# Kernel optimization log

Hardware: AMD Instinct MI355X
Metric: run time of the kernel (lower is better)

## Reference

```python
import jax, jax.numpy as jnp
import numpy as np

B, IN, H, MID = 16384, 256, 512, 64
GRID_SIZE, ORDER = 5, 3
GRID_LO, GRID_HI = -1.0, 1.0
NB = GRID_SIZE + ORDER  # 8 spline basis functions per input feature
LN_EPS = 1e-5


def make_grid(in_features):
    h = (GRID_HI - GRID_LO) / GRID_SIZE
    g = np.arange(-ORDER, GRID_SIZE + ORDER + 1, dtype=np.float32) * h + GRID_LO
    return jnp.asarray(np.tile(g, (in_features, 1)))  # (in, grid_size + 2*order + 1)


def layer_norm(x, g, b):
    mu = jnp.mean(x, axis=-1, keepdims=True)
    var = jnp.var(x, axis=-1, keepdims=True)
    return (x - mu) * jax.lax.rsqrt(var + LN_EPS) * g + b


def b_splines(x, grid):
    # x: (B, in), grid: (in, G). Cox-de Boor recursion (efficient-kan convention).
    xe = x[:, :, None]
    bases = ((xe >= grid[:, :-1]) & (xe < grid[:, 1:])).astype(x.dtype)
    for k in range(1, ORDER + 1):
        left = (xe - grid[:, :-(k + 1)]) / (grid[:, k:-1] - grid[:, :-(k + 1)])
        right = (grid[:, k + 1:] - xe) / (grid[:, k + 1:] - grid[:, 1:-k])
        bases = left * bases[:, :, :-1] + right * bases[:, :, 1:]
    return bases  # (B, in, NB)


def kan_linear(x, base_w, spline_w, scaler, grid):
    # base path: silu(x) @ W_base^T ; spline path: B-spline bases contracted with scaled spline weights
    base = jax.nn.silu(x) @ base_w.T
    bs = b_splines(x, grid)
    spline = jnp.einsum('bik,oik->bo', bs, spline_w * scaler[:, :, None])
    return base + spline


def setup_inputs() -> dict:
    key = jax.random.key(0)
    ks = jax.random.split(key, 24)

    def n(k, shape, fan_in):
        return jax.random.normal(k, shape, dtype=jnp.float32) / np.sqrt(fan_in)

    H2 = 2 * H
    return {
        'x': jax.random.normal(ks[0], (B, IN), jnp.float32),
        'h_prev': jax.random.normal(ks[1], (B, H), jnp.float32),
        'ip_w': n(ks[2], (H, IN), IN), 'ip_b': jnp.zeros((H,), jnp.float32),
        'rg_w': n(ks[3], (H, H2), H2), 'rg_b': jnp.zeros((H,), jnp.float32),
        'rg_g': jnp.ones((H,), jnp.float32), 'rg_beta': jnp.zeros((H,), jnp.float32),
        'ug_w': n(ks[4], (H, H2), H2), 'ug_b': jnp.zeros((H,), jnp.float32),
        'ug_g': jnp.ones((H,), jnp.float32), 'ug_beta': jnp.zeros((H,), jnp.float32),
        'k1_base': n(ks[5], (MID, H2), H2),
        'k1_spline': n(ks[6], (MID, H2, NB), H2) * 0.1,
        'k1_scaler': n(ks[7], (MID, H2), H2) + 1.0,
        'grid1': make_grid(H2),
        'k2_base': n(ks[8], (H, MID), MID),
        'k2_spline': n(ks[9], (H, MID, NB), MID) * 0.1,
        'k2_scaler': n(ks[10], (H, MID), MID) + 1.0,
        'grid2': make_grid(MID),
        'cn_g': jnp.ones((H,), jnp.float32), 'cn_b': jnp.zeros((H,), jnp.float32),
        'rp_w': n(ks[11], (H, H2), H2), 'rp_b': jnp.zeros((H,), jnp.float32),
    }


def reference(x, h_prev, ip_w, ip_b, rg_w, rg_b, rg_g, rg_beta, ug_w, ug_b, ug_g, ug_beta,
              k1_base, k1_spline, k1_scaler, grid1, k2_base, k2_spline, k2_scaler, grid2,
              cn_g, cn_b, rp_w, rp_b):
    x_proj = x @ ip_w.T + ip_b
    combined = jnp.concatenate([x_proj, h_prev], axis=1)  # (B, 2H)
    # reset gate is computed in the original forward but never used; kept for faithfulness
    reset = jnp.tanh(layer_norm(combined @ rg_w.T + rg_b, rg_g, rg_beta))  # noqa: F841
    update = jax.nn.sigmoid(layer_norm(combined @ ug_w.T + ug_b, ug_g, ug_beta))
    # KAN candidate: [2H] -> 64 -> H
    mid = kan_linear(combined, k1_base, k1_spline, k1_scaler, grid1)
    h_cand = kan_linear(mid, k2_base, k2_spline, k2_scaler, grid2)
    residual = combined @ rp_w.T + rp_b
    h_cand = layer_norm(h_cand + residual, cn_g, cn_b)
    h_cand = layer_norm(h_cand, cn_g, cn_b)  # same LayerNorm applied twice, as in source
    h_cand = jax.nn.silu(h_cand)
    h_t = (1.0 - update) * h_prev + update * h_cand
    return h_t
```

## Files before the change

kernel.cpp:

```cpp
#include <hip/hip_runtime.h>
#include <hip/hip_bf16.h>

#define BATCH 16384

typedef __attribute__((ext_vector_type(8))) short short8;
typedef __attribute__((ext_vector_type(4))) float f32x4;

typedef const __attribute__((address_space(1))) uint* gas_t;
typedef __attribute__((address_space(3))) uint* las_t;

__device__ __forceinline__ void gl_lds16(const void* g, void* l) {
    __builtin_amdgcn_global_load_lds((gas_t)g, (las_t)l, 16, 0, 0);
}

__device__ __forceinline__ float bf2f(uint u) { union { uint u; float f; } v; v.u = u << 16; return v.f; }
__device__ __forceinline__ ushort f2bf(float f) {
    union { float f; uint u; } v; v.f = f;
    uint r = v.u + 0x7fffu + ((v.u >> 16) & 1u);
    return (ushort)(r >> 16);
}
__device__ __forceinline__ uint pack2(float a, float b) { return (uint)f2bf(a) | ((uint)f2bf(b) << 16); }
__device__ __forceinline__ uint pack_trunc(float lo, float hi) {
    return __builtin_amdgcn_perm(__float_as_uint(hi), __float_as_uint(lo), 0x07060302u);
}
__device__ __forceinline__ float sigmoidf_(float x) { return __builtin_amdgcn_rcpf(1.0f + __expf(-x)); }
__device__ __forceinline__ float siluf_(float x)    { return x * sigmoidf_(x); }

__device__ __forceinline__ void xcd_swz(int& bm, int& bn) {
    int lin = blockIdx.x + blockIdx.y * 128;
    int c = lin & 7, s = lin >> 3;
    bm = c * 16 + (s >> 2);
    bn = s & 3;
}

__device__ __forceinline__ void bases_packed(float x, float g0, float inv_h, uint o[4]) {
    float u = (x - g0) * inv_h;
    float fl = floorf(u);
    float f = u - fl;
    float f2 = f * f, f3 = f2 * f;
    float Ca = f3 * (1.0f / 6.0f);
    float Cb = (1.0f / 6.0f) + 0.5f * (f + f2 - f3);
    float Cc = (2.0f / 3.0f) + 0.5f * f3 - f2;
    float Cd = (1.0f / 6.0f) + 0.5f * (f2 - f) - f3 * (1.0f / 6.0f);
    int t0 = (int)fl;
    t0 = max(-8, min(t0, 19));
    uint dlo = pack_trunc(Cd, Cc);
    uint dhi = pack_trunc(Cb, Ca);
    unsigned long long D = (unsigned long long)dlo | ((unsigned long long)dhi << 32);
    int sp = t0 * 16 - 48;
    unsigned long long l1 = D << (sp & 63);
    unsigned long long r1 = D >> ((-sp) & 63);
    unsigned long long r2 = D >> ((64 - sp) & 63);
    unsigned long long l2 = D << ((sp - 64) & 63);
    unsigned long long lo = (sp >= 0) ? (sp < 64 ? l1 : 0ull) : (sp > -64 ? r1 : 0ull);
    unsigned long long hi = (sp > 0 && sp < 128) ? (sp < 64 ? r2 : l2) : 0ull;
    o[0] = (uint)lo; o[1] = (uint)(lo >> 32); o[2] = (uint)hi; o[3] = (uint)(hi >> 32);
}

__global__ __launch_bounds__(256) void prep_all(const float* __restrict__ hp,
                                                const float* __restrict__ ip_w, const float* __restrict__ ug_w,
                                                const float* __restrict__ rp,  const float* __restrict__ k2b,
                                                const float* __restrict__ k2s, const float* __restrict__ k2sc,
                                                const float* __restrict__ k1b, const float* __restrict__ k1s,
                                                const float* __restrict__ k1sc,
                                                ushort* __restrict__ acat,
                                                ushort* __restrict__ ipw, ushort* __restrict__ ugw,
                                                ushort* __restrict__ wcat, ushort* __restrict__ w1aug) {
    int t = blockIdx.x * 256 + threadIdx.x;
    if (t < 1048576) {
        int b = t >> 6, j = (t & 63) * 8;
        const float4* s = (const float4*)(hp + (size_t)b * 512 + j);
        float4 a = s[0], c = s[1];
        uint4 o; o.x = pack2(a.x, a.y); o.y = pack2(a.z, a.w); o.z = pack2(c.x, c.y); o.w = pack2(c.z, c.w);
        *(uint4*)(acat + (size_t)b * 1600 + 512 + j) = o;
        return;
    }
    t -= 1048576;
    if (t < 131072) { ipw[t] = f2bf(ip_w[t]); return; }
    t -= 131072;
    if (t < 524288) { ugw[t] = f2bf(ug_w[t]); return; }
    t -= 524288;
    if (t < 819200) {
        int n = t / 1600, c = t % 1600; float v;
        if (c < 1024) v = rp[n * 1024 + c];
        else if (c < 1088) v = k2b[n * 64 + (c - 1024)];
        else { int i = (c - 1088) >> 3, k = (c - 1088) & 7; v = k2s[(n * 64 + i) * 8 + k] * k2sc[n * 64 + i]; }
        wcat[t] = f2bf(v); return;
    }
    t -= 819200;
    if (t < 589824) {
        int n = t / 9216, c = t % 9216; float v;
        if (c < 1024) v = k1b[n * 1024 + c];
        else { int i = (c - 1024) >> 3, k = (c - 1024) & 7; v = k1s[(n * 1024 + i) * 8 + k] * k1sc[n * 1024 + i]; }
        w1aug[t] = f2bf(v);
    }
}

__global__ __launch_bounds__(256) void gemm_mfma(const ushort* __restrict__ A, int lda,
                                                 const ushort* __restrict__ Wt, int ldw,
                                                 const float* __restrict__ bias,
                                                 ushort* __restrict__ C, int ldc, int K) {
    __shared__ ushort As[2][128 * 64];
    __shared__ ushort Bs[2][128 * 64];
    const int tid = threadIdx.x;
    const int w = tid >> 6, lane = tid & 63;
    const int fr = lane & 15, fq = lane >> 4;
    int bm, bn; xcd_swz(bm, bn);
    const int m0 = bm * 128, n0 = bn * 128;
    const int wm = w & 1, wn = w >> 1;

    const int srow8 = lane >> 3;
    const int scol  = ((lane & 7) ^ srow8) << 3;
    const ushort* gA[4]; const ushort* gB[4]; int fa[4];
#pragma unroll
    for (int j = 0; j < 4; ++j) {
        int rowj = (j * 4 + w) * 8 + srow8;
        fa[j] = (j * 4 + w) * 512 + lane * 8;
        gA[j] = A  + (size_t)(m0 + rowj) * lda + scol;
        gB[j] = Wt + (size_t)(n0 + rowj) * ldw + scol;
    }
    const int nt = K / 64;
#pragma unroll
    for (int j = 0; j < 4; ++j) {
        gl_lds16(gA[j], &As[0][fa[j]]); gl_lds16(gB[j], &Bs[0][fa[j]]);
        gA[j] += 64; gB[j] += 64;
    }
    f32x4 acc[4][4] = {};
    int cur = 0;
    for (int t = 0; t < nt; ++t) {
        __syncthreads();
        if (t + 1 < nt) {
#pragma unroll
            for (int j = 0; j < 4; ++j) {
                gl_lds16(gA[j], &As[cur ^ 1][fa[j]]); gl_lds16(gB[j], &Bs[cur ^ 1][fa[j]]);
                gA[j] += 64; gB[j] += 64;
            }
        }
#pragma unroll
        for (int s = 0; s < 2; ++s) {
            const int csw = ((s * 4 + fq) ^ (fr & 7)) << 3;
            short8 af[4], bv[4];
#pragma unroll
            for (int mi = 0; mi < 4; ++mi)
                af[mi] = *(const short8*)(&As[cur][(wm * 64 + mi * 16 + fr) * 64 + csw]);
#pragma unroll
            for (int ni = 0; ni < 4; ++ni)
                bv[ni] = *(const short8*)(&Bs[cur][(wn * 64 + ni * 16 + fr) * 64 + csw]);
#pragma unroll
            for (int mi = 0; mi < 4; ++mi)
#pragma unroll
                for (int ni = 0; ni < 4; ++ni)
                    acc[mi][ni] = __builtin_amdgcn_mfma_f32_16x16x32_bf16(af[mi], bv[ni], acc[mi][ni], 0, 0, 0);
        }
        cur ^= 1;
    }
#pragma unroll
    for (int mi = 0; mi < 4; ++mi) {
#pragma unroll
        for (int ni = 0; ni < 4; ++ni) {
            int n = n0 + wn * 64 + ni * 16 + fr;
            float bvs = bias[n];
#pragma unroll
            for (int r = 0; r < 4; ++r) {
                int m = m0 + wm * 64 + mi * 16 + fq * 4 + r;
                C[(size_t)m * ldc + n] = f2bf(acc[mi][ni][r] + bvs);
            }
        }
    }
}

__global__ __launch_bounds__(256) void gemm_ip(const float* __restrict__ X,
                                               const ushort* __restrict__ Wt,
                                               const float* __restrict__ bias,
                                               ushort* __restrict__ acat) {
    __shared__ ushort As[2][128 * 64];
    __shared__ ushort Bs[2][128 * 64];
    const int tid = threadIdx.x;
    const int w = tid >> 6, lane = tid & 63;
    const int fr = lane & 15, fq = lane >> 4;
    int bm, bn; xcd_swz(bm, bn);
    const int m0 = bm * 128, n0 = bn * 128;
    const int wm = w & 1, wn = w >> 1;

    const int srow8 = lane >> 3;
    const int scol = ((lane & 7) ^ srow8) << 3;
    const ushort* gB[4]; int fa[4];
#pragma unroll
    for (int j = 0; j < 4; ++j) {
        int rowj = (j * 4 + w) * 8 + srow8;
        fa[j] = (j * 4 + w) * 512 + lane * 8;
        gB[j] = Wt + (size_t)(n0 + rowj) * 256 + scol;
    }
    const float* gA[4]; int ar[4];
#pragma unroll
    for (int j = 0; j < 4; ++j) {
        int rj = j * 32 + (tid >> 3);
        int lc = (tid & 7) ^ (rj & 7);
        ar[j] = rj * 64 + (tid & 7) * 8;
        gA[j] = X + (size_t)(m0 + rj) * 256 + lc * 8;
    }
    float4 va[4], vb[4];
#pragma unroll
    for (int j = 0; j < 4; ++j) { gl_lds16(gB[j], &Bs[0][fa[j]]); gB[j] += 64; }
#pragma unroll
    for (int j = 0; j < 4; ++j) { va[j] = *(const float4*)gA[j]; vb[j] = *(const float4*)(gA[j] + 4); gA[j] += 64; }
#pragma unroll
    for (int j = 0; j < 4; ++j) {
        uint4 o; o.x = pack2(va[j].x, va[j].y); o.y = pack2(va[j].z, va[j].w);
        o.z = pack2(vb[j].x, vb[j].y); o.w = pack2(vb[j].z, vb[j].w);
        *(uint4*)&As[0][ar[j]] = o;
    }
    f32x4 acc[4][4] = {};
    int cur = 0;
    for (int t = 0; t < 4; ++t) {
        __syncthreads();
        if (t < 3) {
#pragma unroll
            for (int j = 0; j < 4; ++j) { gl_lds16(gB[j], &Bs[cur ^ 1][fa[j]]); gB[j] += 64; }
#pragma unroll
            for (int j = 0; j < 4; ++j) { va[j] = *(const float4*)gA[j]; vb[j] = *(const float4*)(gA[j] + 4); gA[j] += 64; }
        }
#pragma unroll
        for (int s = 0; s < 2; ++s) {
            const int csw = ((s * 4 + fq) ^ (fr & 7)) << 3;
            short8 af[4], bv[4];
#pragma unroll
            for (int mi = 0; mi < 4; ++mi)
                af[mi] = *(const short8*)(&As[cur][(wm * 64 + mi * 16 + fr) * 64 + csw]);
#pragma unroll
            for (int ni = 0; ni < 4; ++ni)
                bv[ni] = *(const short8*)(&Bs[cur][(wn * 64 + ni * 16 + fr) * 64 + csw]);
#pragma unroll
            for (int mi = 0; mi < 4; ++mi)
#pragma unroll
                for (int ni = 0; ni < 4; ++ni)
                    acc[mi][ni] = __builtin_amdgcn_mfma_f32_16x16x32_bf16(af[mi], bv[ni], acc[mi][ni], 0, 0, 0);
        }
        if (t < 3) {
#pragma unroll
            for (int j = 0; j < 4; ++j) {
                uint4 o; o.x = pack2(va[j].x, va[j].y); o.y = pack2(va[j].z, va[j].w);
                o.z = pack2(vb[j].x, vb[j].y); o.w = pack2(vb[j].z, vb[j].w);
                *(uint4*)&As[cur ^ 1][ar[j]] = o;
            }
        }
        cur ^= 1;
    }
#pragma unroll
    for (int mi = 0; mi < 4; ++mi) {
#pragma unroll
        for (int ni = 0; ni < 4; ++ni) {
            int n = n0 + wn * 64 + ni * 16 + fr;
            float bvs = bias[n];
#pragma unroll
            for (int r = 0; r < 4; ++r) {
                int m = m0 + wm * 64 + mi * 16 + fq * 4 + r;
                acat[(size_t)m * 1600 + n] = f2bf(acc[mi][ni][r] + bvs);
            }
        }
    }
}

__global__ __launch_bounds__(256) void kan1_mfma(const ushort* __restrict__ acat,
                                                 const ushort* __restrict__ w1aug,
                                                 const float* __restrict__ grid1,
                                                 ushort* __restrict__ midp) {
    __shared__ ushort As[2][64 * 64];
    __shared__ ushort Bs[2][64 * 64];
    const int tid = threadIdx.x;
    const int w = tid >> 6, lane = tid & 63;
    const int fr = lane & 15, fq = lane >> 4;
    const int m0 = blockIdx.x * 64;
    const int kb = blockIdx.y;
    const float g0 = grid1[0];
    const float inv_h = 1.0f / (grid1[1] - g0);

    const int srow = tid >> 3, sc = tid & 7;
    const int xr = srow & 7;
    const int lc8 = (sc ^ xr) << 3;
    const ushort* wB0  = w1aug + (size_t)srow * 9216 + lc8;
    const ushort* wB1  = w1aug + (size_t)(srow + 32) * 9216 + lc8;
    const int wpo = srow * 64 + lc8;
    const int wm = w & 1, wn = w >> 1;
    const int cB = kb * 128;
    const int bB = 1024 + kb * 1024;

    const ushort* aR0 = acat + (size_t)(m0 + srow) * 1600;
    const ushort* aR1 = acat + (size_t)(m0 + srow + 32) * 1600;

    uint4 sA0[2], sA1[2];
#pragma unroll
    for (int s = 0; s < 2; ++s) {
        sA0[s] = *(const uint4*)(aR0 + cB + s * 64 + sc * 8);
        sA1[s] = *(const uint4*)(aR1 + cB + s * 64 + sc * 8);
    }
    uint xa[16], xb[16];
#pragma unroll
    for (int bs = 0; bs < 16; ++bs) {
        xa[bs] = aR0[cB + bs * 8 + sc];
        xb[bs] = aR1[cB + bs * 8 + sc];
    }

    f32x4 acc[2][2] = {};
    auto stageB = [&](int c, int buf) {
        gl_lds16(wB0 + c, &Bs[buf][tid * 8]);
        gl_lds16(wB1 + c, &Bs[buf][2048 + tid * 8]);
    };
    auto stageAsilu = [&](int s, int buf) {
        uint r0[4] = {sA0[s].x, sA0[s].y, sA0[s].z, sA0[s].w};
        uint r1[4] = {sA1[s].x, sA1[s].y, sA1[s].z, sA1[s].w};
        uint o0[4], o1[4];
#pragma unroll
        for (int p = 0; p < 4; ++p) {
            o0[p] = pack_trunc(siluf_(bf2f(r0[p] & 0xffffu)), siluf_(bf2f(r0[p] >> 16)));
            o1[p] = pack_trunc(siluf_(bf2f(r1[p] & 0xffffu)), siluf_(bf2f(r1[p] >> 16)));
        }
        uint4 q0; q0.x = o0[0]; q0.y = o0[1]; q0.z = o0[2]; q0.w = o0[3];
        uint4 q1; q1.x = o1[0]; q1.y = o1[1]; q1.z = o1[2]; q1.w = o1[3];
        *(uint4*)&As[buf][wpo] = q0;
        *(uint4*)&As[buf][2048 + wpo] = q1;
    };
    auto stageAbases = [&](uint x0u, uint x1u, int buf) {
        uint o0[4], o1[4];
        bases_packed(bf2f(x0u), g0, inv_h, o0);
        bases_packed(bf2f(x1u), g0, inv_h, o1);
        uint4 q0; q0.x = o0[0]; q0.y = o0[1]; q0.z = o0[2]; q0.w = o0[3];
        uint4 q1; q1.x = o1[0]; q1.y = o1[1]; q1.z = o1[2]; q1.w = o1[3];
        *(uint4*)&As[buf][wpo] = q0;
        *(uint4*)&As[buf][2048 + wpo] = q1;
    };
    auto mfma_step = [&](int buf) {
        __builtin_amdgcn_s_setprio(1);
#pragma unroll
        for (int s2 = 0; s2 < 2; ++s2) {
            short8 af[2], bv[2];
#pragma unroll
            for (int mi = 0; mi < 2; ++mi) {
                int arow = wm * 32 + mi * 16 + fr;
                af[mi] = *(const short8*)(&As[buf][arow * 64 + (((s2 * 4 + fq) ^ (arow & 7)) << 3)]);
            }
#pragma unroll
            for (int ni = 0; ni < 2; ++ni) {
                int brow = wn * 32 + ni * 16 + fr;
                bv[ni] = *(const short8*)(&Bs[buf][brow * 64 + (((s2 * 4 + fq) ^ (brow & 7)) << 3)]);
            }
#pragma unroll
            for (int mi = 0; mi < 2; ++mi)
#pragma unroll
                for (int ni = 0; ni < 2; ++ni)
                    acc[mi][ni] = __builtin_amdgcn_mfma_f32_16x16x32_bf16(af[mi], bv[ni], acc[mi][ni], 0, 0, 0);
        }
        __builtin_amdgcn_s_setprio(0);
    };

    stageB(cB, 0); stageAsilu(0, 0);
    __syncthreads();
    stageB(cB + 64, 1); stageAsilu(1, 1);
    mfma_step(0);
    __syncthreads();
    stageB(bB, 0); stageAbases(xa[0], xb[0], 0);
    mfma_step(1);
#pragma unroll
    for (int bs = 0; bs < 15; ++bs) {
        __syncthreads();
        stageB(bB + (bs + 1) * 64, (bs + 1) & 1);
        stageAbases(xa[bs + 1], xb[bs + 1], (bs + 1) & 1);
        mfma_step(bs & 1);
    }
    __syncthreads();
    mfma_step(1);

    ushort* outp = midp + (size_t)kb * (BATCH * 64);
#pragma unroll
    for (int mi = 0; mi < 2; ++mi)
#pragma unroll
        for (int ni = 0; ni < 2; ++ni)
#pragma unroll
            for (int r = 0; r < 4; ++r)
                outp[(size_t)(m0 + wm * 32 + mi * 16 + fq * 4 + r) * 64 + wn * 32 + ni * 16 + fr] = f2bf(acc[mi][ni][r]);
}

__global__ __launch_bounds__(256) void bs2_kernel(const ushort* __restrict__ midp,
                                                  const float* __restrict__ grid2,
                                                  ushort* __restrict__ acat) {
    int t4 = blockIdx.x * 256 + threadIdx.x;
    if (t4 >= BATCH * 16) return;
    int base = t4 * 4;
    float xs[4] = {0.f, 0.f, 0.f, 0.f};
#pragma unroll
    for (int p = 0; p < 8; ++p) {
        uint2 v = *(const uint2*)(midp + (size_t)p * (BATCH * 64) + base);
        xs[0] += bf2f(v.x & 0xffffu); xs[1] += bf2f(v.x >> 16);
        xs[2] += bf2f(v.y & 0xffffu); xs[3] += bf2f(v.y >> 16);
    }
    int b = base >> 6, i = base & 63;
    float g0 = grid2[0], inv_h = 1.0f / (grid2[1] - g0);
    uint2 sil;
    sil.x = pack2(siluf_(xs[0]), siluf_(xs[1]));
    sil.y = pack2(siluf_(xs[2]), siluf_(xs[3]));
    *(uint2*)&acat[(size_t)b * 1600 + 1024 + i] = sil;
#pragma unroll
    for (int e = 0; e < 4; ++e) {
        uint o[4];
        bases_packed(xs[e], g0, inv_h, o);
        uint4 o4; o4.x = o[0]; o4.y = o[1]; o4.z = o[2]; o4.w = o[3];
        *(uint4*)&acat[(size_t)b * 1600 + 1088 + (i + e) * 8] = o4;
    }
}

__device__ __forceinline__ void block_reduce_2(float& a, float& b, float (*red)[4]) {
#pragma unroll
    for (int off = 32; off; off >>= 1) {
        a += __shfl_xor(a, off, 64);
        b += __shfl_xor(b, off, 64);
    }
    int lane = threadIdx.x & 63, wid = threadIdx.x >> 6;
    if (lane == 0) { red[0][wid] = a; red[1][wid] = b; }
    __syncthreads();
    a = red[0][0] + red[0][1] + red[0][2] + red[0][3];
    b = red[1][0] + red[1][1] + red[1][2] + red[1][3];
}

__global__ __launch_bounds__(256) void final2(const ushort* __restrict__ ug,
                                              const ushort* __restrict__ hcb,
                                              const ushort* __restrict__ acat,
                                              const float* __restrict__ ug_g,
                                              const float* __restrict__ ug_beta,
                                              const float* __restrict__ cg,
                                              const float* __restrict__ cb,
                                              float* __restrict__ out) {
    int row = blockIdx.x, tid = threadIdx.x;
    __shared__ float rA[2][4], rB[2][4], rC[2][4];
    float u0 = bf2f((uint)ug[(size_t)row * 512 + tid]);
    float u1 = bf2f((uint)ug[(size_t)row * 512 + tid + 256]);
    float h0 = bf2f((uint)hcb[(size_t)row * 512 + tid]);
    float h1 = bf2f((uint)hcb[(size_t)row * 512 + tid + 256]);
    float hp0 = bf2f((uint)acat[(size_t)row * 1600 + 512 + tid]);
    float hp1 = bf2f((uint)acat[(size_t)row * 1600 + 768 + tid]);
    float s = u0 + u1, ss = u0 * u0 + u1 * u1;
    block_reduce_2(s, ss, rA);
    float mu = s * (1.0f / 512.0f);
    float var = ss * (1.0f / 512.0f) - mu * mu;
    float r = rsqrtf(var + 1e-5f);
    float uu0 = sigmoidf_((u0 - mu) * r * ug_g[tid] + ug_beta[tid]);
    float uu1 = sigmoidf_((u1 - mu) * r * ug_g[tid + 256] + ug_beta[tid + 256]);
    float cg0 = cg[tid], cg1 = cg[tid + 256], cb0 = cb[tid], cb1 = cb[tid + 256];
    float s2 = h0 + h1, ss2 = h0 * h0 + h1 * h1;
    block_reduce_2(s2, ss2, rB);
    float mu2 = s2 * (1.0f / 512.0f);
    float var2 = ss2 * (1.0f / 512.0f) - mu2 * mu2;
    float r2 = rsqrtf(var2 + 1e-5f);
    float w0 = (h0 - mu2) * r2 * cg0 + cb0;
    float w1 = (h1 - mu2) * r2 * cg1 + cb1;
    float s3 = w0 + w1, ss3 = w0 * w0 + w1 * w1;
    block_reduce_2(s3, ss3, rC);
    float mu3 = s3 * (1.0f / 512.0f);
    float var3 = ss3 * (1.0f / 512.0f) - mu3 * mu3;
    float r3 = rsqrtf(var3 + 1e-5f);
    float c0 = siluf_((w0 - mu3) * r3 * cg0 + cb0);
    float c1 = siluf_((w1 - mu3) * r3 * cg1 + cb1);
    size_t o0 = (size_t)row * 512 + tid, o1 = o0 + 256;
    out[o0] = (1.0f - uu0) * hp0 + uu0 * c0;
    out[o1] = (1.0f - uu1) * hp1 + uu1 * c1;
}

extern "C" void kernel_launch(void* const* d_in, const int* in_sizes, int n_in,
                              void* d_out, int out_size, void* d_ws, size_t ws_size,
                              hipStream_t stream) {
    const float* x        = (const float*)d_in[0];
    const float* h_prev   = (const float*)d_in[1];
    const float* ip_w     = (const float*)d_in[2];
    const float* ip_b     = (const float*)d_in[3];
    const float* ug_w     = (const float*)d_in[8];
    const float* ug_b     = (const float*)d_in[9];
    const float* ug_g     = (const float*)d_in[10];
    const float* ug_beta  = (const float*)d_in[11];
    const float* k1_base  = (const float*)d_in[12];
    const float* k1_spline= (const float*)d_in[13];
    const float* k1_scaler= (const float*)d_in[14];
    const float* grid1    = (const float*)d_in[15];
    const float* k2_base  = (const float*)d_in[16];
    const float* k2_spline= (const float*)d_in[17];
    const float* k2_scaler= (const float*)d_in[18];
    const float* grid2    = (const float*)d_in[19];
    const float* cn_g     = (const float*)d_in[20];
    const float* cn_b     = (const float*)d_in[21];
    const float* rp_w     = (const float*)d_in[22];
    const float* rp_b     = (const float*)d_in[23];
    float* out = (float*)d_out;
    char* W = (char*)d_ws;

    ushort* Acat    = (ushort*)(W);
    ushort* ug_bf   = (ushort*)(W + 52428800);
    ushort* midp    = (ushort*)(W + 69206016);
    ushort* hc_bf   = (ushort*)(W + 102760448);
    ushort* ipw_bf  = (ushort*)(W + 136314880);
    ushort* ugw_bf  = (ushort*)(W + 136577024);
    ushort* wcat    = (ushort*)(W + 137625600);
    ushort* w1aug   = (ushort*)(W + 139264000);

    hipLaunchKernelGGL(prep_all, dim3(12160), dim3(256), 0, stream,
                       h_prev, ip_w, ug_w, rp_w, k2_base, k2_spline, k2_scaler,
                       k1_base, k1_spline, k1_scaler,
                       Acat, ipw_bf, ugw_bf, wcat, w1aug);

    hipLaunchKernelGGL(gemm_ip, dim3(BATCH / 128, 4), dim3(256), 0, stream,
                       x, ipw_bf, ip_b, Acat);

    hipLaunchKernelGGL(gemm_mfma, dim3(BATCH / 128, 4), dim3(256), 0, stream,
                       Acat, 1600, ugw_bf, 1024, ug_b, ug_bf, 512, 1024);

    hipLaunchKernelGGL(kan1_mfma, dim3(BATCH / 64, 8), dim3(256), 0, stream,
                       Acat, w1aug, grid1, midp);
    hipLaunchKernelGGL(bs2_kernel, dim3(BATCH * 16 / 256), dim3(256), 0, stream, midp, grid2, Acat);

    hipLaunchKernelGGL(gemm_mfma, dim3(BATCH / 128, 4), dim3(256), 0, stream,
                       Acat, 1600, wcat, 1600, rp_b, hc_bf, 512, 1600);

    hipLaunchKernelGGL(final2, dim3(BATCH), dim3(256), 0, stream, ug_bf, hc_bf, Acat, ug_g, ug_beta, cn_g, cn_b, out);
}
```

Before: 159.0 us.

## Merge update-gate GEMM into KAN1 kernel as interleaved heterogeneous blocks

Combines the update-gate GEMM launch and the KAN layer-1 kernel into a single launch of 2560 blocks. Every fifth block computes a 128x128 update-gate tile and the rest compute KAN1 tiles, so both independent workloads share the GPU concurrently and one launch is removed. The gate path inlines the GEMM loop with an LDS layout of 32-element rows, and the block-index remapping has to cover both work sets exactly. Mixing block types may cause load imbalance and register or LDS pressure set by the heavier path.

Measured after the change: 175.6 us. 10.4% more time.

```diff
diff --git a/kernel.cpp b/kernel.cpp
--- a/kernel.cpp
+++ b/kernel.cpp
@@ -261,27 +261,89 @@
     }
 }
 
-__global__ __launch_bounds__(256) void kan1_mfma(const ushort* __restrict__ acat,
-                                                 const ushort* __restrict__ w1aug,
-                                                 const float* __restrict__ grid1,
-                                                 ushort* __restrict__ midp) {
-    __shared__ ushort As[2][64 * 64];
-    __shared__ ushort Bs[2][64 * 64];
+__global__ __launch_bounds__(256) void kan1_ug(const ushort* __restrict__ acat,
+                                               const ushort* __restrict__ w1aug,
+                                               const float* __restrict__ grid1,
+                                               ushort* __restrict__ midp,
+                                               const ushort* __restrict__ ugw,
+                                               const float* __restrict__ ug_b,
+                                               ushort* __restrict__ ug_bf) {
+    __shared__ ushort As[2][4096];
+    __shared__ ushort Bs[2][4096];
     const int tid = threadIdx.x;
+    const int lin = blockIdx.x;
     const int w = tid >> 6, lane = tid & 63;
     const int fr = lane & 15, fq = lane >> 4;
-    const int m0 = blockIdx.x * 64;
-    const int kb = blockIdx.y;
+    const int wm = w & 1, wn = w >> 1;
+
+    if (lin % 5 == 0) {
+        const int g = lin / 5;
+        const int m0 = (g & 127) * 128, n0 = (g >> 7) * 128;
+        const int r0 = tid >> 2, r1 = 64 + (tid >> 2), pc = tid & 3;
+        const int lc0 = (pc ^ ((r0 >> 1) & 3)) << 3;
+        const int lc1 = (pc ^ ((r1 >> 1) & 3)) << 3;
+        const int fa0 = tid * 8, fa1 = (tid + 256) * 8;
+        const ushort* gA0 = acat + (size_t)(m0 + r0) * 1600 + lc0;
+        const ushort* gA1 = acat + (size_t)(m0 + r1) * 1600 + lc1;
+        const ushort* gB0 = ugw  + (size_t)(n0 + r0) * 1024 + lc0;
+        const ushort* gB1 = ugw  + (size_t)(n0 + r1) * 1024 + lc1;
+        gl_lds16(gA0, &As[0][fa0]); gl_lds16(gA1, &As[0][fa1]);
+        gl_lds16(gB0, &Bs[0][fa0]); gl_lds16(gB1, &Bs[0][fa1]);
+        gA0 += 32; gA1 += 32; gB0 += 32; gB1 += 32;
+        f32x4 acc[4][4] = {};
+        int cur = 0;
+        for (int t = 0; t < 32; ++t) {
+            __syncthreads();
+            if (t + 1 < 32) {
+                gl_lds16(gA0, &As[cur ^ 1][fa0]); gl_lds16(gA1, &As[cur ^ 1][fa1]);
+                gl_lds16(gB0, &Bs[cur ^ 1][fa0]); gl_lds16(gB1, &Bs[cur ^ 1][fa1]);
+                gA0 += 32; gA1 += 32; gB0 += 32; gB1 += 32;
+            }
+            short8 af[4], bv[4];
+#pragma unroll
+            for (int mi = 0; mi < 4; ++mi) {
+                int row = wm * 64 + mi * 16 + fr;
+                af[mi] = *(const short8*)(&As[cur][row * 32 + ((fq ^ ((row >> 1) & 3)) << 3)]);
+            }
+#pragma unroll
+            for (int ni = 0; ni < 4; ++ni) {
+                int row = wn * 64 + ni * 16 + fr;
+                bv[ni] = *(const short8*)(&Bs[cur][row * 32 + ((fq ^ ((row >> 1) & 3)) << 3)]);
+            }
+#pragma unroll
+            for (int mi = 0; mi < 4; ++mi)
+#pragma unroll
+                for (int ni = 0; ni < 4; ++ni)
+                    acc[mi][ni] = __builtin_amdgcn_mfma_f32_16x16x32_bf16(af[mi], bv[ni], acc[mi][ni], 0, 0, 0);
+            cur ^= 1;
+        }
+#pragma unroll
+        for (int mi = 0; mi < 4; ++mi) {
+#pragma unroll
+            for (int ni = 0; ni < 4; ++ni) {
+                int n = n0 + wn * 64 + ni * 16 + fr;
+                float bvs = ug_b[n];
+#pragma unroll
+                for (int r = 0; r < 4; ++r) {
+                    int m = m0 + wm * 64 + mi * 16 + fq * 4 + r;
+                    ug_bf[(size_t)m * 512 + n] = f2bf(acc[mi][ni][r] + bvs);
+                }
+            }
+        }
+        return;
+    }
+
+    const int id = lin - 1 - lin / 5;
+    const int m0 = (id & 255) * 64;
+    const int kb = id >> 8;
     const float g0 = grid1[0];
     const float inv_h = 1.0f / (grid1[1] - g0);
 
     const int srow = tid >> 3, sc = tid & 7;
-    const int xr = srow & 7;
-    const int lc8 = (sc ^ xr) << 3;
+    const int lc8 = (sc ^ (srow & 7)) << 3;
     const ushort* wB0  = w1aug + (size_t)srow * 9216 + lc8;
     const ushort* wB1  = w1aug + (size_t)(srow + 32) * 9216 + lc8;
     const int wpo = srow * 64 + lc8;
-    const int wm = w & 1, wn = w >> 1;
     const int cB = kb * 128;
     const int bB = 1024 + kb * 1024;
 
@@ -507,11 +569,9 @@
     hipLaunchKernelGGL(gemm_ip, dim3(BATCH / 128, 4), dim3(256), 0, stream,
                        x, ipw_bf, ip_b, Acat);
 
-    hipLaunchKernelGGL(gemm_mfma, dim3(BATCH / 128, 4), dim3(256), 0, stream,
-                       Acat, 1600, ugw_bf, 1024, ug_b, ug_bf, 512, 1024);
-
-    hipLaunchKernelGGL(kan1_mfma, dim3(BATCH / 64, 8), dim3(256), 0, stream,
-                       Acat, w1aug, grid1, midp);
+    hipLaunchKernelGGL(kan1_ug, dim3(2560), dim3(256), 0, stream,
+                       Acat, w1aug, grid1, midp, ugw_bf, ug_b, ug_bf);
+
     hipLaunchKernelGGL(bs2_kernel, dim3(BATCH * 16 / 256), dim3(256), 0, stream, midp, grid2, Acat);
 
     hipLaunchKernelGGL(gemm_mfma, dim3(BATCH / 128, 4), dim3(256), 0, stream,
```
